# Optimization experiments

Hardware: AMD Instinct MI355X
Metric: run time of the kernel (lower is better)

The kernel has to match this reference:

```python
import jax, jax.numpy as jnp
import numpy as np

N = 4096

def setup_inputs() -> dict:
    key = jax.random.key(0)
    kA, kB = jax.random.split(key)
    A = jnp.tril(jax.random.normal(kA, (N, N), dtype=jnp.float32))
    B = jnp.tril(jax.random.normal(kB, (N, N), dtype=jnp.float32))
    return {"A": A, "B": B}

def reference(A, B):
    # Product of two lower-triangular matrices; result is lower-triangular.
    # tril applied to the dense matmul reproduces the intended math exactly
    # (and zeroes any numerical noise in the structural-zero upper triangle).
    return jnp.tril(jnp.matmul(A, B))
```

## Files before the change

### kernel.cpp

```cpp
#include <hip/hip_runtime.h>
#include <stdint.h>

#define NN 4096
#define NB2 16
#define BK 64

#define NUNITS 260
#define ZBASE 260
#define TGRID 380
#define NSPLIT 78
#define NWSLOTS 202

#define PGRID_W 8192
#define PGRID_A 8504

typedef __bf16 bf16x8 __attribute__((ext_vector_type(8)));
typedef float f32x4 __attribute__((ext_vector_type(4)));
typedef unsigned short ushort8 __attribute__((ext_vector_type(8)));

__device__ __forceinline__ unsigned short f2bf(float x) {
    union { float f; unsigned int u; } v; v.f = x;
    unsigned int u = v.u;
    u += 0x7fffu + ((u >> 16) & 1u);
    return (unsigned short)(u >> 16);
}

#define GLOAD16(g, l) __builtin_amdgcn_global_load_lds( \
    (const __attribute__((address_space(1))) unsigned int*)(g), \
    (__attribute__((address_space(3))) unsigned int*)(l), 16, 0, 0)

__device__ __forceinline__ void split_decode(int z, int& bi, int& bj, int& nu, int& u0) {
    int d = 15, acc = 0;
    for (;;) {
        nu = (d + 4) >> 2;
        int cnt = NB2 - d;
        if (z < cnt) { bj = z; bi = z + d; u0 = acc + z * nu; return; }
        z -= cnt; acc += cnt * nu; --d;
    }
}

__global__ __launch_bounds__(256) void prep(const float* __restrict__ A,
                                            const float* __restrict__ B,
                                            unsigned short* __restrict__ Ab,
                                            unsigned short* __restrict__ Bt,
                                            float* __restrict__ C) {
    __shared__ float tile[64][65];
    int bid = blockIdx.x;
    int tid = threadIdx.x;

    if (bid < 4096) {
        int i = bid;
        int nslots = ((i >> 8) + 1) * 32;
        const float4* src = reinterpret_cast<const float4*>(A + (size_t)i * NN);
        unsigned short* dst = Ab + (size_t)i * NN;
        for (int p = tid; p < nslots; p += 256) {
            float4 x0 = src[p * 2], x1 = src[p * 2 + 1];
            ushort8 o;
            o[0] = f2bf(x0.x); o[1] = f2bf(x0.y); o[2] = f2bf(x0.z); o[3] = f2bf(x0.w);
            o[4] = f2bf(x1.x); o[5] = f2bf(x1.y); o[6] = f2bf(x1.z); o[7] = f2bf(x1.w);
            *reinterpret_cast<ushort8*>(dst + p * 8) = o;
        }
        return;
    }
    if (bid < 8192) {
        int s = bid - 4096;
        int n64 = s >> 6, k64 = s & 63;
        if (k64 < (n64 & ~3)) return;
        int n0 = n64 * 64, k0 = k64 * 64;
        int tx = tid & 63, ty = tid >> 6;
#pragma unroll
        for (int r = 0; r < 16; ++r) {
            int k = ty + r * 4;
            tile[k][tx] = B[(size_t)(k0 + k) * NN + n0 + tx];
        }
        __syncthreads();
#pragma unroll
        for (int r = 0; r < 16; ++r) {
            int n = ty + r * 4;
            Bt[(size_t)(n0 + n) * NN + k0 + tx] = f2bf(tile[tx][n]);
        }
        return;
    }
    {
        int z = bid - 8192;
        int bi, bj, nu, u0; split_decode(z >> 2, bi, bj, nu, u0);
        int part = z & 3;
        float4 zf = make_float4(0.f, 0.f, 0.f, 0.f);
        float4* cp = reinterpret_cast<float4*>(C + (size_t)(bi * 256 + part * 64) * NN + (size_t)bj * 256);
#pragma unroll
        for (int i2 = 0; i2 < 16; ++i2) {
            int slot = tid + i2 * 256;
            int row = slot >> 6, c4 = slot & 63;
            cp[(size_t)row * (NN / 4) + c4] = zf;
        }
    }
}

__global__ __launch_bounds__(512, 1) void trimm(const unsigned short* __restrict__ Ab,
                                                const unsigned short* __restrict__ Bt,
                                                float* __restrict__ C,
                                                float* __restrict__ W,
                                                int useW) {
    int bid = blockIdx.x;
    int tid = threadIdx.x;
    int lane = tid & 63;
    int w = tid >> 6;

    if (bid >= ZBASE) {
        int r = bid - ZBASE, bi = 0;
        while (r >= NB2 - 1 - bi) { r -= NB2 - 1 - bi; ++bi; }
        int bj = bi + 1 + r;
        float4 z = make_float4(0.f, 0.f, 0.f, 0.f);
        float4* cp = reinterpret_cast<float4*>(C + (size_t)bi * 256 * NN + (size_t)bj * 256);
#pragma unroll
        for (int i2 = 0; i2 < 32; ++i2) {
            int slot = tid + i2 * 512;
            int row = slot >> 6, c4 = slot & 63;
            cp[(size_t)row * (NN / 4) + c4] = z;
        }
        return;
    }

    int bi, bj, k_lo, nt;
    bool atom;
    {
        int r = bid, d = 15, nu;
        for (;;) {
            nu = (d + 4) >> 2;
            int cnt = (NB2 - d) * nu;
            if (r < cnt) break;
            r -= cnt; --d;
        }
        int t = r / nu, part = r - t * nu;
        bj = t; bi = t + d;
        atom = (nu > 1);
        int ntk = 4 * (d + 1);
        int ntb = ntk / nu, rem = ntk % nu;
        nt = ntb + (part < rem ? 1 : 0);
        int skip = part * ntb + (part < rem ? part : rem);
        k_lo = bj * 256 + skip * BK;
    }
    int k_hi = k_lo + nt * BK;

    __shared__ unsigned short As[4][128 * 64];
    __shared__ unsigned short Bs[4][128 * 64];

    int qwr = w >> 2;
    int qwc = w & 3;
    int fr = lane & 15;
    int c0 = (((lane >> 4) ^ (lane & 7)) * 8);
    int c1 = ((((lane >> 4) | 4) ^ (lane & 7)) * 8);

    int srow = tid >> 3;
    int schunk = ((tid & 7) ^ (srow & 7)) * 8;
    const unsigned short* gA = Ab + (size_t)(bi * 256 + srow) * NN + schunk;
    const unsigned short* gB = Bt + (size_t)(bj * 256 + srow) * NN + schunk;

    f32x4 acc[4][4][2];
#pragma unroll
    for (int q = 0; q < 4; ++q)
#pragma unroll
        for (int m = 0; m < 4; ++m)
#pragma unroll
            for (int n = 0; n < 2; ++n)
                acc[q][m][n] = (f32x4){0.f, 0.f, 0.f, 0.f};

    bf16x8 a0[4], a1[4], bA0[2], bA1[2], bB0[2], bB1[2];

#define STG(XS, gX, h, slot, kk) do { \
        unsigned short* d_ = &XS[slot][0] + tid * 8; \
        GLOAD16(gX + (size_t)(h) * 128 * NN + (kk), d_); \
        GLOAD16(gX + (size_t)((h) * 128 + 64) * NN + (kk), d_ + 4096); \
    } while (0)

#define LDA(slot) do { \
        _Pragma("unroll") for (int m_ = 0; m_ < 4; ++m_) { \
            int r_ = (qwr * 64 + m_ * 16 + fr) * 64; \
            a0[m_] = *reinterpret_cast<const bf16x8*>(&As[slot][r_ + c0]); \
            a1[m_] = *reinterpret_cast<const bf16x8*>(&As[slot][r_ + c1]); \
        } \
    } while (0)

#define LDB(slot, B0V, B1V) do { \
        _Pragma("unroll") for (int n_ = 0; n_ < 2; ++n_) { \
            int r_ = (qwc * 32 + n_ * 16 + fr) * 64; \
            B0V[n_] = *reinterpret_cast<const bf16x8*>(&Bs[slot][r_ + c0]); \
            B1V[n_] = *reinterpret_cast<const bf16x8*>(&Bs[slot][r_ + c1]); \
        } \
    } while (0)

#define MFMAQ(Q, B0V, B1V) do { \
        _Pragma("unroll") for (int m_ = 0; m_ < 4; ++m_) \
        _Pragma("unroll") for (int n_ = 0; n_ < 2; ++n_) { \
            acc[Q][m_][n_] = __builtin_amdgcn_mfma_f32_16x16x32_bf16(a0[m_], B0V[n_], acc[Q][m_][n_], 0, 0, 0); \
            acc[Q][m_][n_] = __builtin_amdgcn_mfma_f32_16x16x32_bf16(a1[m_], B1V[n_], acc[Q][m_][n_], 0, 0, 0); \
        } \
    } while (0)

#define VMC4 asm volatile("s_waitcnt vmcnt(4)" ::: "memory")
#define BAR __builtin_amdgcn_s_barrier()

    STG(As, gA, 0, 0, k_lo);
    STG(Bs, gB, 0, 0, k_lo);
    STG(Bs, gB, 1, 1, k_lo);
    STG(As, gA, 1, 1, k_lo);
    VMC4; BAR;

    for (int t = 0; t < nt; ++t) {
        int p = (t & 1) << 1;
        int np = p ^ 2;
        int kkn = (t + 1 < nt) ? (k_lo + (t + 1) * BK) : k_lo;

        LDA(p); LDB(p, bA0, bA1);
        STG(As, gA, 0, np, kkn);
        BAR;
        __builtin_amdgcn_s_setprio(1); MFMAQ(0, bA0, bA1); __builtin_amdgcn_s_setprio(0);
        VMC4; BAR;

        LDB(p | 1, bB0, bB1);
        STG(Bs, gB, 0, np, kkn);
        BAR;
        __builtin_amdgcn_s_setprio(1); MFMAQ(1, bB0, bB1); __builtin_amdgcn_s_setprio(0);
        VMC4; BAR;

        LDA(p | 1);
        STG(Bs, gB, 1, np | 1, kkn);
        BAR;
        __builtin_amdgcn_s_setprio(1); MFMAQ(2, bB0, bB1); __builtin_amdgcn_s_setprio(0);
        BAR;

        STG(As, gA, 1, np | 1, kkn);
        BAR;
        __builtin_amdgcn_s_setprio(1); MFMAQ(3, bA0, bA1); __builtin_amdgcn_s_setprio(0);
        VMC4; BAR;
    }
    asm volatile("s_waitcnt vmcnt(0)" ::: "memory");
#undef STG
#undef LDA
#undef LDB
#undef MFMAQ
#undef VMC4
#undef BAR

    int r4 = (lane >> 4) * 4;
    if (atom && useW) {
        float* wb = W + (size_t)bid * 65536;
#pragma unroll
        for (int q = 0; q < 4; ++q) {
            int mh = q >> 1, nh = ((q + 1) >> 1) & 1;
#pragma unroll
            for (int m = 0; m < 4; ++m)
#pragma unroll
                for (int n = 0; n < 2; ++n) {
                    int row = mh * 128 + qwr * 64 + m * 16 + r4;
                    int col = nh * 128 + qwc * 32 + n * 16 + fr;
                    float* wp = wb + (size_t)row * 256 + col;
#pragma unroll
                    for (int r2 = 0; r2 < 4; ++r2)
                        wp[r2 * 256] = acc[q][m][n][r2];
                }
        }
    } else if (atom) {
#pragma unroll
        for (int q = 0; q < 4; ++q) {
            int mh = q >> 1, nh = ((q + 1) >> 1) & 1;
#pragma unroll
            for (int m = 0; m < 4; ++m)
#pragma unroll
                for (int n = 0; n < 2; ++n) {
                    int row = bi * 256 + mh * 128 + qwr * 64 + m * 16 + r4;
                    int col = bj * 256 + nh * 128 + qwc * 32 + n * 16 + fr;
                    float* cp = C + (size_t)row * NN + col;
#pragma unroll
                    for (int r2 = 0; r2 < 4; ++r2)
                        atomicAdd(&cp[(size_t)r2 * NN], acc[q][m][n][r2]);
                }
        }
    } else {
#pragma unroll
        for (int q = 0; q < 4; ++q) {
            int mh = q >> 1, nh = ((q + 1) >> 1) & 1;
#pragma unroll
            for (int m = 0; m < 4; ++m)
#pragma unroll
                for (int n = 0; n < 2; ++n) {
                    int row = bi * 256 + mh * 128 + qwr * 64 + m * 16 + r4;
                    int col = bj * 256 + nh * 128 + qwc * 32 + n * 16 + fr;
                    float* cp = C + (size_t)row * NN + col;
#pragma unroll
                    for (int r2 = 0; r2 < 4; ++r2)
                        cp[(size_t)r2 * NN] = acc[q][m][n][r2];
                }
        }
    }
}

__global__ __launch_bounds__(512) void merge(const float* __restrict__ W,
                                             float* __restrict__ C) {
    int z = blockIdx.x;
    int tid = threadIdx.x;
    int bi, bj, nu, u0; split_decode(z, bi, bj, nu, u0);
    const float4* w0 = reinterpret_cast<const float4*>(W + (size_t)u0 * 65536);
#pragma unroll 4
    for (int it = 0; it < 32; ++it) {
        int s = tid + it * 512;
        int row = s >> 6, c4 = s & 63;
        float4 a = w0[s];
        for (int p = 1; p < nu; ++p) {
            float4 b = w0[(size_t)p * 16384 + s];
            a.x += b.x; a.y += b.y; a.z += b.z; a.w += b.w;
        }
        float4* cp = reinterpret_cast<float4*>(C) + (size_t)(bi * 256 + row) * (NN / 4) + bj * 64 + c4;
        *cp = a;
    }
}

extern "C" void kernel_launch(void* const* d_in, const int* in_sizes, int n_in,
                              void* d_out, int out_size, void* d_ws, size_t ws_size,
                              hipStream_t stream) {
    const float* A = (const float*)d_in[0];
    const float* B = (const float*)d_in[1];
    float* C = (float*)d_out;
    unsigned short* Ab = (unsigned short*)d_ws;
    unsigned short* Bt = Ab + (size_t)NN * NN;
    const size_t base = (size_t)2 * NN * NN * sizeof(unsigned short);
    const size_t wbytes = (size_t)NWSLOTS * 65536 * sizeof(float);
    const int useW = (ws_size >= base + wbytes) ? 1 : 0;
    float* W = (float*)((char*)d_ws + base);

    prep<<<useW ? PGRID_W : PGRID_A, 256, 0, stream>>>(A, B, Ab, Bt, C);
    trimm<<<TGRID, 512, 0, stream>>>(Ab, Bt, C, W, useW);
    if (useW) merge<<<NSPLIT, 512, 0, stream>>>(W, C);
}
```

Measured before the change: 92.08 us.

## Replace workspace split-K merge with two-way split and atomic accumulation

Changes split-K work decomposition so only diagonals with d>=8 are split in two (instead of up to four parts), cutting work units from 260 to 172. The workspace-buffer path and the separate merge kernel are removed; split partials are now always added atomically into C, which prep zeroes. This drops a kernel launch and the extra write/read of partial tiles, at the cost of fewer workgroups (less CU fill on 256 CUs), larger per-unit load imbalance, and atomic add traffic.

```diff
diff --git a/kernel.cpp b/kernel.cpp
--- a/kernel.cpp
+++ b/kernel.cpp
@@ -5,14 +5,11 @@
 #define NB2 16
 #define BK 64
 
-#define NUNITS 260
-#define ZBASE 260
-#define TGRID 380
-#define NSPLIT 78
-#define NWSLOTS 202
-
-#define PGRID_W 8192
-#define PGRID_A 8504
+#define NUNITS 172
+#define ZBASE 172
+#define TGRID 292
+
+#define PGRID 8336
 
 typedef __bf16 bf16x8 __attribute__((ext_vector_type(8)));
 typedef float f32x4 __attribute__((ext_vector_type(4)));
@@ -29,14 +26,10 @@
     (const __attribute__((address_space(1))) unsigned int*)(g), \
     (__attribute__((address_space(3))) unsigned int*)(l), 16, 0, 0)
 
-__device__ __forceinline__ void split_decode(int z, int& bi, int& bj, int& nu, int& u0) {
-    int d = 15, acc = 0;
-    for (;;) {
-        nu = (d + 4) >> 2;
-        int cnt = NB2 - d;
-        if (z < cnt) { bj = z; bi = z + d; u0 = acc + z * nu; return; }
-        z -= cnt; acc += cnt * nu; --d;
-    }
+__device__ __forceinline__ void split_map(int z, int& bi, int& bj) {
+    int d = 15;
+    while (z >= NB2 - d) { z -= NB2 - d; --d; }
+    bj = z; bi = z + d;
 }
 
 __global__ __launch_bounds__(256) void prep(const float* __restrict__ A,
@@ -82,9 +75,9 @@
         return;
     }
     {
-        int z = bid - 8192;
-        int bi, bj, nu, u0; split_decode(z >> 2, bi, bj, nu, u0);
-        int part = z & 3;
+        int zb = bid - 8192;
+        int bi, bj; split_map(zb >> 2, bi, bj);
+        int part = zb & 3;
         float4 zf = make_float4(0.f, 0.f, 0.f, 0.f);
         float4* cp = reinterpret_cast<float4*>(C + (size_t)(bi * 256 + part * 64) * NN + (size_t)bj * 256);
 #pragma unroll
@@ -98,9 +91,7 @@
 
 __global__ __launch_bounds__(512, 1) void trimm(const unsigned short* __restrict__ Ab,
                                                 const unsigned short* __restrict__ Bt,
-                                                float* __restrict__ C,
-                                                float* __restrict__ W,
-                                                int useW) {
+                                                float* __restrict__ C) {
     int bid = blockIdx.x;
     int tid = threadIdx.x;
     int lane = tid & 63;
@@ -126,21 +117,20 @@
     {
         int r = bid, d = 15, nu;
         for (;;) {
-            nu = (d + 4) >> 2;
+            nu = (d >= 8) ? 2 : 1;
             int cnt = (NB2 - d) * nu;
             if (r < cnt) break;
             r -= cnt; --d;
         }
         int t = r / nu, part = r - t * nu;
         bj = t; bi = t + d;
-        atom = (nu > 1);
+        atom = (nu == 2);
         int ntk = 4 * (d + 1);
-        int ntb = ntk / nu, rem = ntk % nu;
-        nt = ntb + (part < rem ? 1 : 0);
-        int skip = part * ntb + (part < rem ? part : rem);
-        k_lo = bj * 256 + skip * BK;
+        nt = ntk / nu;
+        k_lo = bj * 256 + part * nt * BK;
     }
     int k_hi = k_lo + nt * BK;
+    (void)k_hi;
 
     __shared__ unsigned short As[4][128 * 64];
     __shared__ unsigned short Bs[4][128 * 64];
@@ -243,24 +233,7 @@
 #undef BAR
 
     int r4 = (lane >> 4) * 4;
-    if (atom && useW) {
-        float* wb = W + (size_t)bid * 65536;
-#pragma unroll
-        for (int q = 0; q < 4; ++q) {
-            int mh = q >> 1, nh = ((q + 1) >> 1) & 1;
-#pragma unroll
-            for (int m = 0; m < 4; ++m)
-#pragma unroll
-                for (int n = 0; n < 2; ++n) {
-                    int row = mh * 128 + qwr * 64 + m * 16 + r4;
-                    int col = nh * 128 + qwc * 32 + n * 16 + fr;
-                    float* wp = wb + (size_t)row * 256 + col;
-#pragma unroll
-                    for (int r2 = 0; r2 < 4; ++r2)
-                        wp[r2 * 256] = acc[q][m][n][r2];
-                }
-        }
-    } else if (atom) {
+    if (atom) {
 #pragma unroll
         for (int q = 0; q < 4; ++q) {
             int mh = q >> 1, nh = ((q + 1) >> 1) & 1;
@@ -292,26 +265,6 @@
                         cp[(size_t)r2 * NN] = acc[q][m][n][r2];
                 }
         }
-    }
-}
-
-__global__ __launch_bounds__(512) void merge(const float* __restrict__ W,
-                                             float* __restrict__ C) {
-    int z = blockIdx.x;
-    int tid = threadIdx.x;
-    int bi, bj, nu, u0; split_decode(z, bi, bj, nu, u0);
-    const float4* w0 = reinterpret_cast<const float4*>(W + (size_t)u0 * 65536);
-#pragma unroll 4
-    for (int it = 0; it < 32; ++it) {
-        int s = tid + it * 512;
-        int row = s >> 6, c4 = s & 63;
-        float4 a = w0[s];
-        for (int p = 1; p < nu; ++p) {
-            float4 b = w0[(size_t)p * 16384 + s];
-            a.x += b.x; a.y += b.y; a.z += b.z; a.w += b.w;
-        }
-        float4* cp = reinterpret_cast<float4*>(C) + (size_t)(bi * 256 + row) * (NN / 4) + bj * 64 + c4;
-        *cp = a;
     }
 }
 
@@ -323,12 +276,6 @@
     float* C = (float*)d_out;
     unsigned short* Ab = (unsigned short*)d_ws;
     unsigned short* Bt = Ab + (size_t)NN * NN;
-    const size_t base = (size_t)2 * NN * NN * sizeof(unsigned short);
-    const size_t wbytes = (size_t)NWSLOTS * 65536 * sizeof(float);
-    const int useW = (ws_size >= base + wbytes) ? 1 : 0;
-    float* W = (float*)((char*)d_ws + base);
-
-    prep<<<useW ? PGRID_W : PGRID_A, 256, 0, stream>>>(A, B, Ab, Bt, C);
-    trimm<<<TGRID, 512, 0, stream>>>(Ab, Bt, C, W, useW);
-    if (useW) merge<<<NSPLIT, 512, 0, stream>>>(W, C);
-}
+    prep<<<PGRID, 256, 0, stream>>>(A, B, Ab, Bt, C);
+    trimm<<<TGRID, 512, 0, stream>>>(Ab, Bt, C);
+}
```

New measurement: 80.38 us. 12.7% less time.

## Restructure GEMM main loop to two barriered phases and widen merge grid

Applied to the files above, without the earlier changes.

The trimm inner loop drops from eight barriers per K-step to two. Each phase loads A plus both B halves from shared memory and issues two MFMA quadrants, then launches the global-to-LDS prefetches for the next stage. This cuts synchronization stalls and keeps more MFMA work between barriers, but holds more B fragments in registers and relies on looser vmcnt waits. The merge kernel is also split into 8 sub-blocks per tile with 256 threads, giving more parallelism for the reduction.

```diff
diff --git a/kernel.cpp b/kernel.cpp
--- a/kernel.cpp
+++ b/kernel.cpp
@@ -140,7 +140,6 @@
         int skip = part * ntb + (part < rem ? part : rem);
         k_lo = bj * 256 + skip * BK;
     }
-    int k_hi = k_lo + nt * BK;
 
     __shared__ unsigned short As[4][128 * 64];
     __shared__ unsigned short Bs[4][128 * 64];
@@ -165,7 +164,7 @@
             for (int n = 0; n < 2; ++n)
                 acc[q][m][n] = (f32x4){0.f, 0.f, 0.f, 0.f};
 
-    bf16x8 a0[4], a1[4], bA0[2], bA1[2], bB0[2], bB1[2];
+    bf16x8 a0[4], a1[4], bh0c0[2], bh0c1[2], bh1c0[2], bh1c1[2];
 
 #define STG(XS, gX, h, slot, kk) do { \
         unsigned short* d_ = &XS[slot][0] + tid * 8; \
@@ -173,15 +172,15 @@
         GLOAD16(gX + (size_t)((h) * 128 + 64) * NN + (kk), d_ + 4096); \
     } while (0)
 
-#define LDA(slot) do { \
+#define LDAH(slot, AV0, AV1) do { \
         _Pragma("unroll") for (int m_ = 0; m_ < 4; ++m_) { \
             int r_ = (qwr * 64 + m_ * 16 + fr) * 64; \
-            a0[m_] = *reinterpret_cast<const bf16x8*>(&As[slot][r_ + c0]); \
-            a1[m_] = *reinterpret_cast<const bf16x8*>(&As[slot][r_ + c1]); \
+            AV0[m_] = *reinterpret_cast<const bf16x8*>(&As[slot][r_ + c0]); \
+            AV1[m_] = *reinterpret_cast<const bf16x8*>(&As[slot][r_ + c1]); \
         } \
     } while (0)
 
-#define LDB(slot, B0V, B1V) do { \
+#define LDBH(slot, B0V, B1V) do { \
         _Pragma("unroll") for (int n_ = 0; n_ < 2; ++n_) { \
             int r_ = (qwc * 32 + n_ * 16 + fr) * 64; \
             B0V[n_] = *reinterpret_cast<const bf16x8*>(&Bs[slot][r_ + c0]); \
@@ -189,57 +188,53 @@
         } \
     } while (0)
 
-#define MFMAQ(Q, B0V, B1V) do { \
+#define MFMAQ(Q, AV0, AV1, B0V, B1V) do { \
         _Pragma("unroll") for (int m_ = 0; m_ < 4; ++m_) \
         _Pragma("unroll") for (int n_ = 0; n_ < 2; ++n_) { \
-            acc[Q][m_][n_] = __builtin_amdgcn_mfma_f32_16x16x32_bf16(a0[m_], B0V[n_], acc[Q][m_][n_], 0, 0, 0); \
-            acc[Q][m_][n_] = __builtin_amdgcn_mfma_f32_16x16x32_bf16(a1[m_], B1V[n_], acc[Q][m_][n_], 0, 0, 0); \
+            acc[Q][m_][n_] = __builtin_amdgcn_mfma_f32_16x16x32_bf16(AV0[m_], B0V[n_], acc[Q][m_][n_], 0, 0, 0); \
+            acc[Q][m_][n_] = __builtin_amdgcn_mfma_f32_16x16x32_bf16(AV1[m_], B1V[n_], acc[Q][m_][n_], 0, 0, 0); \
         } \
     } while (0)
 
-#define VMC4 asm volatile("s_waitcnt vmcnt(4)" ::: "memory")
 #define BAR __builtin_amdgcn_s_barrier()
 
     STG(As, gA, 0, 0, k_lo);
     STG(Bs, gB, 0, 0, k_lo);
     STG(Bs, gB, 1, 1, k_lo);
     STG(As, gA, 1, 1, k_lo);
-    VMC4; BAR;
 
     for (int t = 0; t < nt; ++t) {
         int p = (t & 1) << 1;
         int np = p ^ 2;
         int kkn = (t + 1 < nt) ? (k_lo + (t + 1) * BK) : k_lo;
 
-        LDA(p); LDB(p, bA0, bA1);
+        asm volatile("s_waitcnt vmcnt(2)" ::: "memory");
+        BAR;
+        LDAH(p, a0, a1);
+        LDBH(p, bh0c0, bh0c1);
+        LDBH(p | 1, bh1c0, bh1c1);
+        __builtin_amdgcn_s_setprio(1);
+        MFMAQ(0, a0, a1, bh0c0, bh0c1);
+        MFMAQ(1, a0, a1, bh1c0, bh1c1);
+        __builtin_amdgcn_s_setprio(0);
         STG(As, gA, 0, np, kkn);
+        STG(Bs, gB, 0, np, kkn);
+
+        asm volatile("s_waitcnt vmcnt(4)" ::: "memory");
         BAR;
-        __builtin_amdgcn_s_setprio(1); MFMAQ(0, bA0, bA1); __builtin_amdgcn_s_setprio(0);
-        VMC4; BAR;
-
-        LDB(p | 1, bB0, bB1);
-        STG(Bs, gB, 0, np, kkn);
-        BAR;
-        __builtin_amdgcn_s_setprio(1); MFMAQ(1, bB0, bB1); __builtin_amdgcn_s_setprio(0);
-        VMC4; BAR;
-
-        LDA(p | 1);
+        LDAH(p | 1, a0, a1);
+        __builtin_amdgcn_s_setprio(1);
+        MFMAQ(2, a0, a1, bh1c0, bh1c1);
+        MFMAQ(3, a0, a1, bh0c0, bh0c1);
+        __builtin_amdgcn_s_setprio(0);
         STG(Bs, gB, 1, np | 1, kkn);
-        BAR;
-        __builtin_amdgcn_s_setprio(1); MFMAQ(2, bB0, bB1); __builtin_amdgcn_s_setprio(0);
-        BAR;
-
         STG(As, gA, 1, np | 1, kkn);
-        BAR;
-        __builtin_amdgcn_s_setprio(1); MFMAQ(3, bA0, bA1); __builtin_amdgcn_s_setprio(0);
-        VMC4; BAR;
     }
     asm volatile("s_waitcnt vmcnt(0)" ::: "memory");
 #undef STG
-#undef LDA
-#undef LDB
+#undef LDAH
+#undef LDBH
 #undef MFMAQ
-#undef VMC4
 #undef BAR
 
     int r4 = (lane >> 4) * 4;
@@ -295,22 +290,25 @@
     }
 }
 
-__global__ __launch_bounds__(512) void merge(const float* __restrict__ W,
+__global__ __launch_bounds__(256) void merge(const float* __restrict__ W,
                                              float* __restrict__ C) {
-    int z = blockIdx.x;
+    int blk = blockIdx.x;
+    int z = blk >> 3;
+    int sub = blk & 7;
     int tid = threadIdx.x;
     int bi, bj, nu, u0; split_decode(z, bi, bj, nu, u0);
-    const float4* w0 = reinterpret_cast<const float4*>(W + (size_t)u0 * 65536);
-#pragma unroll 4
-    for (int it = 0; it < 32; ++it) {
-        int s = tid + it * 512;
+    const float4* w0 = reinterpret_cast<const float4*>(W + (size_t)u0 * 65536) + sub * 2048;
+#pragma unroll 2
+    for (int it = 0; it < 8; ++it) {
+        int s = tid + it * 256;
         int row = s >> 6, c4 = s & 63;
         float4 a = w0[s];
         for (int p = 1; p < nu; ++p) {
             float4 b = w0[(size_t)p * 16384 + s];
             a.x += b.x; a.y += b.y; a.z += b.z; a.w += b.w;
         }
-        float4* cp = reinterpret_cast<float4*>(C) + (size_t)(bi * 256 + row) * (NN / 4) + bj * 64 + c4;
+        float4* cp = reinterpret_cast<float4*>(C) +
+                     (size_t)(bi * 256 + sub * 32 + row) * (NN / 4) + bj * 64 + c4;
         *cp = a;
     }
 }
@@ -330,5 +328,5 @@
 
     prep<<<useW ? PGRID_W : PGRID_A, 256, 0, stream>>>(A, B, Ab, Bt, C);
     trimm<<<TGRID, 512, 0, stream>>>(Ab, Bt, C, W, useW);
-    if (useW) merge<<<NSPLIT, 512, 0, stream>>>(W, C);
-}
+    if (useW) merge<<<NSPLIT * 8, 256, 0, stream>>>(W, C);
+}
```

After: 76.75 us. -16.6%, faster.
